# Optimization experiments

Measured on AMD Instinct MI355X. Metric: run time of the kernel, lower is better.

The kernel has to match this reference:

```python
import jax, jax.numpy as jnp
import numpy as np

RADIUS = 2.0
DECAY = 1.0


def setup_inputs() -> dict:
    key = jax.random.key(0)
    k1, k2 = jax.random.split(key)
    x = jax.random.normal(k1, (2048, 16), dtype=jnp.float32)
    data = jax.random.normal(k2, (65536, 16), dtype=jnp.float32)
    return {"x": x, "data": data}


def reference(x, data):
    # Brute-force L2 nearest-neighbor (faiss IndexFlatL2 / IVF nlist=1 == exact search)
    # dist2[q, n] = ||x_q - data_n||^2, via the expansion trick.
    x2 = jnp.sum(x * x, axis=1, keepdims=True)            # [Nq, 1]
    d2 = jnp.sum(data * data, axis=1)                      # [Nd]
    dist2 = x2 + d2[None, :] - 2.0 * (x @ data.T)          # [Nq, Nd] -- dominant traffic
    nn2 = jnp.maximum(jnp.min(dist2, axis=1), 0.0)         # clamp tiny negatives from cancellation
    dist = jnp.sqrt(jnp.maximum(nn2, 1e-12))               # sqrt of squared L2, squeeze(k=1)

    # bump_above(dist, RADIUS, DECAY):
    #   inside mask: exp(decay / (d^2 - r^2)) / exp(-decay / r^2)
    #   outside: 0
    r2 = RADIUS * RADIUS
    mask = jnp.abs(dist) < RADIUS
    denom = jnp.where(mask, dist * dist - r2, -1.0)        # safe denom outside mask
    bump = jnp.where(mask, jnp.exp(DECAY / denom + DECAY / r2), 0.0)
    return bump
```

## Files before the change

### kernel.cpp

```cpp
#include <hip/hip_runtime.h>
#include <float.h>
#include <math.h>

constexpr int NQ = 2048;
constexpr int ND = 65536;
constexpr int D  = 16;

constexpr int SCH   = 64;
constexpr int CP    = ND / SCH;
constexpr int TPW   = CP / 32;
constexpr int NPAIR = TPW / 2;

typedef short bf16x8 __attribute__((ext_vector_type(8)));
typedef float f32x16 __attribute__((ext_vector_type(16)));

__device__ __forceinline__ unsigned short f2bf(float f) {
    unsigned u = __float_as_uint(f);
    u += 0x7FFFu + ((u >> 16) & 1u);
    return (unsigned short)(u >> 16);
}
__device__ __forceinline__ float bf2f(unsigned short h) {
    return __uint_as_float(((unsigned)h) << 16);
}

__global__ __launch_bounds__(256) void pack_data(const float* __restrict__ data,
                                                 unsigned short* __restrict__ Ppk,
                                                 float* __restrict__ nhf) {
    const int p = blockIdx.x * 256 + threadIdx.x;
    const float4* r4 = (const float4*)(data + (size_t)p * D);
    float4 a = r4[0], b = r4[1], c = r4[2], e = r4[3];
    float v[16] = {a.x, a.y, a.z, a.w, b.x, b.y, b.z, b.w,
                   c.x, c.y, c.z, c.w, e.x, e.y, e.z, e.w};
    unsigned short hi[16], lo[16];
    float n = 0.f;
#pragma unroll
    for (int k = 0; k < 16; ++k) {
        n = fmaf(v[k], v[k], n);
        unsigned short h = f2bf(v[k]);
        hi[k] = h;
        lo[k] = f2bf(v[k] - bf2f(h));
    }
    const int t  = p >> 5;
    const int cc = p & 31;
    unsigned short* tb = Ppk + (size_t)t * 1024;
    const uint4* h4 = (const uint4*)hi;
    const uint4* l4 = (const uint4*)lo;
    *(uint4*)(tb +        cc * 8) = h4[0];
    *(uint4*)(tb + 256 +  cc * 8) = h4[1];
    *(uint4*)(tb + 512 +  cc * 8) = l4[0];
    *(uint4*)(tb + 768 +  cc * 8) = l4[1];
    nhf[p] = -0.5f * n;
}

__global__ __launch_bounds__(256, 2) void knn_mfma(const float* __restrict__ x,
                                                   const unsigned short* __restrict__ Ppk,
                                                   const float* __restrict__ nhf,
                                                   float* __restrict__ part) {
    const int tid  = threadIdx.x;
    const int w    = tid >> 6;
    const int l    = tid & 63;
    const int half = l >> 5;
    const int n31  = l & 31;
    const int qbase = blockIdx.x * 256 + w * 64;
    const int pbase = blockIdx.y * CP;

    bf16x8 axh0, axl0, axh1, axl1;
    {
        const float* xr0 = x + (size_t)(qbase + n31) * D + half * 8;
        float4 a0 = *(const float4*)xr0;
        float4 a1 = *(const float4*)(xr0 + 4);
        const float xv0[8] = {a0.x, a0.y, a0.z, a0.w, a1.x, a1.y, a1.z, a1.w};
#pragma unroll
        for (int k = 0; k < 8; ++k) {
            unsigned short h = f2bf(xv0[k]);
            axh0[k] = (short)h;
            axl0[k] = (short)f2bf(xv0[k] - bf2f(h));
        }
        const float* xr1 = x + (size_t)(qbase + 32 + n31) * D + half * 8;
        float4 b0 = *(const float4*)xr1;
        float4 b1 = *(const float4*)(xr1 + 4);
        const float xv1[8] = {b0.x, b0.y, b0.z, b0.w, b1.x, b1.y, b1.z, b1.w};
#pragma unroll
        for (int k = 0; k < 8; ++k) {
            unsigned short h = f2bf(xv1[k]);
            axh1[k] = (short)h;
            axl1[k] = (short)f2bf(xv1[k] - bf2f(h));
        }
    }

    const unsigned short* bp = Ppk + (size_t)(pbase >> 5) * 1024 + l * 8;
    const float*          np = nhf + pbase + n31;

#define LDH(t) (*(const bf16x8*)(bp + (size_t)(t) * 1024))
#define LDL(t) (*(const bf16x8*)(bp + (size_t)(t) * 1024 + 512))
#define LDN(t) (np[(size_t)(t) * 32])

    f32x16 rbest0, rbest1;
#pragma unroll
    for (int r = 0; r < 16; ++r) { rbest0[r] = -FLT_MAX; rbest1[r] = -FLT_MAX; }

    auto compute_pair = [&](bf16x8 h0, bf16x8 l0, float n0,
                            bf16x8 h1, bf16x8 l1, float n1) {
        f32x16 c00, c01, c10, c11;
#pragma unroll
        for (int r = 0; r < 16; ++r) {
            c00[r] = n0; c01[r] = n1; c10[r] = n0; c11[r] = n1;
        }
        c00 = __builtin_amdgcn_mfma_f32_32x32x16_bf16(axh0, h0, c00, 0, 0, 0);
        c01 = __builtin_amdgcn_mfma_f32_32x32x16_bf16(axh0, h1, c01, 0, 0, 0);
        c10 = __builtin_amdgcn_mfma_f32_32x32x16_bf16(axh1, h0, c10, 0, 0, 0);
        c11 = __builtin_amdgcn_mfma_f32_32x32x16_bf16(axh1, h1, c11, 0, 0, 0);
        c00 = __builtin_amdgcn_mfma_f32_32x32x16_bf16(axl0, h0, c00, 0, 0, 0);
        c01 = __builtin_amdgcn_mfma_f32_32x32x16_bf16(axl0, h1, c01, 0, 0, 0);
        c10 = __builtin_amdgcn_mfma_f32_32x32x16_bf16(axl1, h0, c10, 0, 0, 0);
        c11 = __builtin_amdgcn_mfma_f32_32x32x16_bf16(axl1, h1, c11, 0, 0, 0);
        c00 = __builtin_amdgcn_mfma_f32_32x32x16_bf16(axh0, l0, c00, 0, 0, 0);
        c01 = __builtin_amdgcn_mfma_f32_32x32x16_bf16(axh0, l1, c01, 0, 0, 0);
        c10 = __builtin_amdgcn_mfma_f32_32x32x16_bf16(axh1, l0, c10, 0, 0, 0);
        c11 = __builtin_amdgcn_mfma_f32_32x32x16_bf16(axh1, l1, c11, 0, 0, 0);
#pragma unroll
        for (int r = 0; r < 16; ++r) {
            rbest0[r] = fmaxf(rbest0[r], fmaxf(c00[r], c01[r]));
            rbest1[r] = fmaxf(rbest1[r], fmaxf(c10[r], c11[r]));
        }
    };

    bf16x8 Ah0 = LDH(0), Al0 = LDL(0), Ah1 = LDH(1), Al1 = LDL(1);
    float  An0 = LDN(0), An1 = LDN(1);
    bf16x8 Bh0, Bl0, Bh1, Bl1;
    float  Bn0, Bn1;

    for (int p = 0; p < NPAIR; p += 2) {
        const int tB = (p + 1) * 2;
        Bh0 = LDH(tB);     Bl0 = LDL(tB);     Bn0 = LDN(tB);
        Bh1 = LDH(tB + 1); Bl1 = LDL(tB + 1); Bn1 = LDN(tB + 1);
        compute_pair(Ah0, Al0, An0, Ah1, Al1, An1);
        if (p + 2 < NPAIR) {
            const int tA = (p + 2) * 2;
            Ah0 = LDH(tA);     Al0 = LDL(tA);     An0 = LDN(tA);
            Ah1 = LDH(tA + 1); Al1 = LDL(tA + 1); An1 = LDN(tA + 1);
        }
        compute_pair(Bh0, Bl0, Bn0, Bh1, Bl1, Bn1);
    }
#undef LDH
#undef LDL
#undef LDN

#pragma unroll
    for (int r = 0; r < 16; ++r) {
        float v0 = rbest0[r];
        v0 = fmaxf(v0, __shfl_xor(v0, 1, 32));
        v0 = fmaxf(v0, __shfl_xor(v0, 2, 32));
        v0 = fmaxf(v0, __shfl_xor(v0, 4, 32));
        v0 = fmaxf(v0, __shfl_xor(v0, 8, 32));
        v0 = fmaxf(v0, __shfl_xor(v0, 16, 32));
        rbest0[r] = v0;
        float v1 = rbest1[r];
        v1 = fmaxf(v1, __shfl_xor(v1, 1, 32));
        v1 = fmaxf(v1, __shfl_xor(v1, 2, 32));
        v1 = fmaxf(v1, __shfl_xor(v1, 4, 32));
        v1 = fmaxf(v1, __shfl_xor(v1, 8, 32));
        v1 = fmaxf(v1, __shfl_xor(v1, 16, 32));
        rbest1[r] = v1;
    }
    if (n31 == 0) {
        float* pp = part + (size_t)blockIdx.y * NQ + qbase + 4 * half;
#pragma unroll
        for (int r = 0; r < 16; ++r) pp[(r & 3) + 8 * (r >> 2)] = rbest0[r];
        pp += 32;
#pragma unroll
        for (int r = 0; r < 16; ++r) pp[(r & 3) + 8 * (r >> 2)] = rbest1[r];
    }
}

__global__ __launch_bounds__(256) void knn_final(const float* __restrict__ x,
                                                 const float* __restrict__ part,
                                                 float* __restrict__ out) {
    const int q = blockIdx.x * 256 + threadIdx.x;
    const float4* xr = (const float4*)(x + (size_t)q * D);
    float4 a = xr[0], b = xr[1], c = xr[2], e = xr[3];
    float x2 = a.x * a.x;
    x2 = fmaf(a.y, a.y, x2); x2 = fmaf(a.z, a.z, x2); x2 = fmaf(a.w, a.w, x2);
    x2 = fmaf(b.x, b.x, x2); x2 = fmaf(b.y, b.y, x2); x2 = fmaf(b.z, b.z, x2); x2 = fmaf(b.w, b.w, x2);
    x2 = fmaf(c.x, c.x, x2); x2 = fmaf(c.y, c.y, x2); x2 = fmaf(c.z, c.z, x2); x2 = fmaf(c.w, c.w, x2);
    x2 = fmaf(e.x, e.x, x2); x2 = fmaf(e.y, e.y, x2); x2 = fmaf(e.z, e.z, x2); x2 = fmaf(e.w, e.w, x2);

    float mbest = -FLT_MAX;
#pragma unroll
    for (int cI = 0; cI < SCH; ++cI) mbest = fmaxf(mbest, part[(size_t)cI * NQ + q]);

    float nn2  = fmaxf(fmaf(-2.f, mbest, x2), 0.f);
    float dist = sqrtf(fmaxf(nn2, 1e-12f));
    float bump = 0.f;
    if (dist < 2.0f) {
        float denom = dist * dist - 4.0f;
        bump = expf(1.0f / denom + 0.25f);
    }
    out[q] = bump;
}

__global__ __launch_bounds__(256) void neg_half_norms(const float* __restrict__ data,
                                                      float* __restrict__ nhn) {
    const int p = blockIdx.x * 256 + threadIdx.x;
    const float4* r = (const float4*)(data + (size_t)p * D);
    float4 a = r[0], b = r[1], c = r[2], e = r[3];
    float n = a.x * a.x;
    n = fmaf(a.y, a.y, n); n = fmaf(a.z, a.z, n); n = fmaf(a.w, a.w, n);
    n = fmaf(b.x, b.x, n); n = fmaf(b.y, b.y, n); n = fmaf(b.z, b.z, n); n = fmaf(b.w, b.w, n);
    n = fmaf(c.x, c.x, n); n = fmaf(c.y, c.y, n); n = fmaf(c.z, c.z, n); n = fmaf(c.w, c.w, n);
    n = fmaf(e.x, e.x, n); n = fmaf(e.y, e.y, n); n = fmaf(e.z, e.z, n); n = fmaf(e.w, e.w, n);
    nhn[p] = -0.5f * n;
}

__global__ __launch_bounds__(256) void knn_partial_fb(const float* __restrict__ x,
                                                      const float* __restrict__ data,
                                                      const float* __restrict__ nhn,
                                                      float* __restrict__ part, int cp) {
    const int q     = blockIdx.x * 256 + threadIdx.x;
    const int pbase = blockIdx.y * cp;
    const float4* xr = (const float4*)(x + (size_t)q * D);
    const float4 xa = xr[0], xb = xr[1], xc = xr[2], xd = xr[3];
    const float* dp = data + (size_t)pbase * D;
    const float* np = nhn + pbase;
    float best = -FLT_MAX;
    for (int i = 0; i < cp; i += 4) {
#pragma unroll
        for (int j = 0; j < 4; ++j) {
            const float* r  = dp + (size_t)(i + j) * D;
            const float  hn = np[i + j];
            float ca = xa.x * r[0];
            ca = fmaf(xa.y, r[1], ca);  ca = fmaf(xa.z, r[2], ca);  ca = fmaf(xa.w, r[3], ca);
            ca = fmaf(xb.x, r[4], ca);  ca = fmaf(xb.y, r[5], ca);  ca = fmaf(xb.z, r[6], ca);
            ca = fmaf(xb.w, r[7], ca);
            float cb = fmaf(xc.x, r[8], hn);
            cb = fmaf(xc.y, r[9],  cb); cb = fmaf(xc.z, r[10], cb); cb = fmaf(xc.w, r[11], cb);
            cb = fmaf(xd.x, r[12], cb); cb = fmaf(xd.y, r[13], cb); cb = fmaf(xd.z, r[14], cb);
            cb = fmaf(xd.w, r[15], cb);
            best = fmaxf(best, ca + cb);
        }
    }
    part[(size_t)blockIdx.y * NQ + q] = best;
}

__global__ __launch_bounds__(256) void knn_final_fb(const float* __restrict__ x,
                                                    const float* __restrict__ part,
                                                    float* __restrict__ out, int S) {
    const int q = blockIdx.x * 256 + threadIdx.x;
    const float4* xr = (const float4*)(x + (size_t)q * D);
    float4 a = xr[0], b = xr[1], c = xr[2], e = xr[3];
    float x2 = a.x * a.x;
    x2 = fmaf(a.y, a.y, x2); x2 = fmaf(a.z, a.z, x2); x2 = fmaf(a.w, a.w, x2);
    x2 = fmaf(b.x, b.x, x2); x2 = fmaf(b.y, b.y, x2); x2 = fmaf(b.z, b.z, x2); x2 = fmaf(b.w, b.w, x2);
    x2 = fmaf(c.x, c.x, x2); x2 = fmaf(c.y, c.y, x2); x2 = fmaf(c.z, c.z, x2); x2 = fmaf(c.w, c.w, x2);
    x2 = fmaf(e.x, e.x, x2); x2 = fmaf(e.y, e.y, x2); x2 = fmaf(e.z, e.z, x2); x2 = fmaf(e.w, e.w, x2);
    float mb = -FLT_MAX;
    for (int cI = 0; cI < S; ++cI) mb = fmaxf(mb, part[(size_t)cI * NQ + q]);
    float nn2  = fmaxf(fmaf(-2.f, mb, x2), 0.f);
    float dist = sqrtf(fmaxf(nn2, 1e-12f));
    float bump = 0.f;
    if (dist < 2.0f) {
        float denom = dist * dist - 4.0f;
        bump = expf(1.0f / denom + 0.25f);
    }
    out[q] = bump;
}

extern "C" void kernel_launch(void* const* d_in, const int* in_sizes, int n_in,
                              void* d_out, int out_size, void* d_ws, size_t ws_size,
                              hipStream_t stream) {
    const float* x    = (const float*)d_in[0];
    const float* data = (const float*)d_in[1];
    float* out = (float*)d_out;

    const size_t off_nhf  = (size_t)ND * 32 * 2;
    const size_t off_part = off_nhf + (size_t)ND * 4;
    const size_t needed   = off_part + (size_t)SCH * NQ * 4;

    if (ws_size >= needed) {
        unsigned short* Ppk = (unsigned short*)d_ws;
        float* nhf  = (float*)((char*)d_ws + off_nhf);
        float* part = (float*)((char*)d_ws + off_part);

        pack_data<<<ND / 256, 256, 0, stream>>>(data, Ppk, nhf);
        knn_mfma<<<dim3(NQ / 256, SCH), 256, 0, stream>>>(x, Ppk, nhf, part);
        knn_final<<<NQ / 256, 256, 0, stream>>>(x, part, out);
    } else {
        int S = 32;
        while (S > 1 && (size_t)(ND + S * NQ) * sizeof(float) > ws_size) S >>= 1;
        const int cp = ND / S;
        float* nhn  = (float*)d_ws;
        float* part = (float*)d_ws + ND;
        neg_half_norms<<<ND / 256, 256, 0, stream>>>(data, nhn);
        knn_partial_fb<<<dim3(NQ / 256, S), 256, 0, stream>>>(x, data, nhn, part, cp);
        knn_final_fb<<<NQ / 256, 256, 0, stream>>>(x, part, out, S);
    }
}
```

Before: 82.37 us.

## Fuse final reduction into MFMA kernel via atomic max and last-block epilogue

```diff
diff --git a/kernel.cpp b/kernel.cpp
--- a/kernel.cpp
+++ b/kernel.cpp
@@ -23,10 +23,23 @@
     return __uint_as_float(((unsigned)h) << 16);
 }
 
+__device__ __forceinline__ unsigned fkey(float f) {
+    unsigned b = __float_as_uint(f);
+    return (b & 0x80000000u) ? ~b : (b | 0x80000000u);
+}
+__device__ __forceinline__ float funkey(unsigned u) {
+    unsigned b = (u & 0x80000000u) ? (u & 0x7FFFFFFFu) : ~u;
+    return __uint_as_float(b);
+}
+
 __global__ __launch_bounds__(256) void pack_data(const float* __restrict__ data,
                                                  unsigned short* __restrict__ Ppk,
-                                                 float* __restrict__ nhf) {
+                                                 float* __restrict__ nhf,
+                                                 unsigned* __restrict__ bestk,
+                                                 unsigned* __restrict__ cnt) {
     const int p = blockIdx.x * 256 + threadIdx.x;
+    if (blockIdx.x < NQ / 256) bestk[p] = 0u;
+    if (p < NQ / 256) cnt[p] = 0u;
     const float4* r4 = (const float4*)(data + (size_t)p * D);
     float4 a = r4[0], b = r4[1], c = r4[2], e = r4[3];
     float v[16] = {a.x, a.y, a.z, a.w, b.x, b.y, b.z, b.w,
@@ -55,7 +68,9 @@
 __global__ __launch_bounds__(256, 2) void knn_mfma(const float* __restrict__ x,
                                                    const unsigned short* __restrict__ Ppk,
                                                    const float* __restrict__ nhf,
-                                                   float* __restrict__ part) {
+                                                   unsigned* __restrict__ bestk,
+                                                   unsigned* __restrict__ cnt,
+                                                   float* __restrict__ out) {
     const int tid  = threadIdx.x;
     const int w    = tid >> 6;
     const int l    = tid & 63;
@@ -164,39 +179,43 @@
         rbest1[r] = v1;
     }
     if (n31 == 0) {
-        float* pp = part + (size_t)blockIdx.y * NQ + qbase + 4 * half;
-#pragma unroll
-        for (int r = 0; r < 16; ++r) pp[(r & 3) + 8 * (r >> 2)] = rbest0[r];
-        pp += 32;
-#pragma unroll
-        for (int r = 0; r < 16; ++r) pp[(r & 3) + 8 * (r >> 2)] = rbest1[r];
-    }
-}
-
-__global__ __launch_bounds__(256) void knn_final(const float* __restrict__ x,
-                                                 const float* __restrict__ part,
-                                                 float* __restrict__ out) {
-    const int q = blockIdx.x * 256 + threadIdx.x;
-    const float4* xr = (const float4*)(x + (size_t)q * D);
-    float4 a = xr[0], b = xr[1], c = xr[2], e = xr[3];
-    float x2 = a.x * a.x;
-    x2 = fmaf(a.y, a.y, x2); x2 = fmaf(a.z, a.z, x2); x2 = fmaf(a.w, a.w, x2);
-    x2 = fmaf(b.x, b.x, x2); x2 = fmaf(b.y, b.y, x2); x2 = fmaf(b.z, b.z, x2); x2 = fmaf(b.w, b.w, x2);
-    x2 = fmaf(c.x, c.x, x2); x2 = fmaf(c.y, c.y, x2); x2 = fmaf(c.z, c.z, x2); x2 = fmaf(c.w, c.w, x2);
-    x2 = fmaf(e.x, e.x, x2); x2 = fmaf(e.y, e.y, x2); x2 = fmaf(e.z, e.z, x2); x2 = fmaf(e.w, e.w, x2);
-
-    float mbest = -FLT_MAX;
-#pragma unroll
-    for (int cI = 0; cI < SCH; ++cI) mbest = fmaxf(mbest, part[(size_t)cI * NQ + q]);
-
-    float nn2  = fmaxf(fmaf(-2.f, mbest, x2), 0.f);
-    float dist = sqrtf(fmaxf(nn2, 1e-12f));
-    float bump = 0.f;
-    if (dist < 2.0f) {
-        float denom = dist * dist - 4.0f;
-        bump = expf(1.0f / denom + 0.25f);
-    }
-    out[q] = bump;
+        unsigned* bq = bestk + qbase + 4 * half;
+#pragma unroll
+        for (int r = 0; r < 16; ++r)
+            atomicMax(&bq[(r & 3) + 8 * (r >> 2)], fkey(rbest0[r]));
+        bq += 32;
+#pragma unroll
+        for (int r = 0; r < 16; ++r)
+            atomicMax(&bq[(r & 3) + 8 * (r >> 2)], fkey(rbest1[r]));
+    }
+
+    __shared__ int lastFlag;
+    __threadfence();
+    __syncthreads();
+    if (tid == 0)
+        lastFlag = (atomicAdd(&cnt[blockIdx.x], 1u) == SCH - 1);
+    __syncthreads();
+    if (lastFlag) {
+        __threadfence();
+        const int q = blockIdx.x * 256 + tid;
+        float mbest = funkey(__hip_atomic_load(&bestk[q], __ATOMIC_RELAXED,
+                                               __HIP_MEMORY_SCOPE_AGENT));
+        const float4* xr = (const float4*)(x + (size_t)q * D);
+        float4 a = xr[0], b = xr[1], c = xr[2], e = xr[3];
+        float x2 = a.x * a.x;
+        x2 = fmaf(a.y, a.y, x2); x2 = fmaf(a.z, a.z, x2); x2 = fmaf(a.w, a.w, x2);
+        x2 = fmaf(b.x, b.x, x2); x2 = fmaf(b.y, b.y, x2); x2 = fmaf(b.z, b.z, x2); x2 = fmaf(b.w, b.w, x2);
+        x2 = fmaf(c.x, c.x, x2); x2 = fmaf(c.y, c.y, x2); x2 = fmaf(c.z, c.z, x2); x2 = fmaf(c.w, c.w, x2);
+        x2 = fmaf(e.x, e.x, x2); x2 = fmaf(e.y, e.y, x2); x2 = fmaf(e.z, e.z, x2); x2 = fmaf(e.w, e.w, x2);
+        float nn2  = fmaxf(fmaf(-2.f, mbest, x2), 0.f);
+        float dist = sqrtf(fmaxf(nn2, 1e-12f));
+        float bump = 0.f;
+        if (dist < 2.0f) {
+            float denom = dist * dist - 4.0f;
+            bump = expf(1.0f / denom + 0.25f);
+        }
+        out[q] = bump;
+    }
 }
 
 __global__ __launch_bounds__(256) void neg_half_norms(const float* __restrict__ data,
@@ -273,17 +292,18 @@
     float* out = (float*)d_out;
 
     const size_t off_nhf  = (size_t)ND * 32 * 2;
-    const size_t off_part = off_nhf + (size_t)ND * 4;
-    const size_t needed   = off_part + (size_t)SCH * NQ * 4;
+    const size_t off_best = off_nhf + (size_t)ND * 4;
+    const size_t off_cnt  = off_best + (size_t)NQ * 4;
+    const size_t needed   = off_cnt + 64;
 
     if (ws_size >= needed) {
         unsigned short* Ppk = (unsigned short*)d_ws;
-        float* nhf  = (float*)((char*)d_ws + off_nhf);
-        float* part = (float*)((char*)d_ws + off_part);
-
-        pack_data<<<ND / 256, 256, 0, stream>>>(data, Ppk, nhf);
-        knn_mfma<<<dim3(NQ / 256, SCH), 256, 0, stream>>>(x, Ppk, nhf, part);
-        knn_final<<<NQ / 256, 256, 0, stream>>>(x, part, out);
+        float*    nhf   = (float*)((char*)d_ws + off_nhf);
+        unsigned* bestk = (unsigned*)((char*)d_ws + off_best);
+        unsigned* cnt   = (unsigned*)((char*)d_ws + off_cnt);
+
+        pack_data<<<ND / 256, 256, 0, stream>>>(data, Ppk, nhf, bestk, cnt);
+        knn_mfma<<<dim3(NQ / 256, SCH), 256, 0, stream>>>(x, Ppk, nhf, bestk, cnt, out);
     } else {
         int S = 32;
         while (S > 1 && (size_t)(ND + S * NQ) * sizeof(float) > ws_size) S >>= 1;
```

After: 111.3 us. +35.1%, slower.
